# Kernel optimization log

Hardware: AMD Instinct MI355X
Metric: run time of the kernel (lower is better)

Reference implementation:

```python
import jax, jax.numpy as jnp
from jax import lax
import numpy as np

B, S, T = 64, 256, 256          # sentences, tokens, parser transitions per sentence
WDIMS, PDIMS = 128, 32
H = 256                          # per-direction hidden = ldims // 2
LDIMS = 2 * H
HID = 512
NRELS = 46
K, NNVECS = 3, 3
SLOTS = (K + 1) * NNVECS         # 12 gathered hidden vectors per transition
FEAT = LDIMS * SLOTS             # 6144 = hidLayer input dim
VW, VP = 40003, 53
ROUT = 2 * NRELS + 1             # 93


def _lstm(x, Wih, Whh, bih, bhh, reverse=False):
    """torch.nn.LSTMCell recurrence over seq axis. x: [B,S,D] -> h: [B,S,H]."""
    Bx = x.shape[0]
    Hh = Whh.shape[1]
    xs = jnp.swapaxes(x, 0, 1)  # [S,B,D]
    xg = xs @ Wih.T + (bih + bhh)  # precompute input gates [S,B,4H]

    def step(carry, g_in):
        h, c = carry
        g = g_in + h @ Whh.T
        i, f, gg, o = jnp.split(g, 4, axis=-1)
        i = jax.nn.sigmoid(i); f = jax.nn.sigmoid(f)
        gg = jnp.tanh(gg); o = jax.nn.sigmoid(o)
        c = f * c + i * gg
        h = o * jnp.tanh(c)
        return (h, c), h

    init = (jnp.zeros((Bx, Hh), x.dtype), jnp.zeros((Bx, Hh), x.dtype))
    _, hs = lax.scan(step, init, xg, reverse=reverse)
    return jnp.swapaxes(hs, 0, 1)  # [B,S,H], backward pass aligned to positions


def _forward(word_ids, pos_ids, feat_idx, wlookup, plookup,
             Wih1f, Whh1f, bih1f, bhh1f, Wih1b, Whh1b, bih1b, bhh1b,
             Wih2f, Whh2f, bih2f, bhh2f, Wih2b, Whh2b, bih2b, bhh2b,
             hidLayer, hidBias, outLayer, outBias,
             rhidLayer, rhidBias, routLayer, routBias):
    # token embeddings: ivec = cat(wordvec, posvec)
    ivec = jnp.concatenate([wlookup[word_ids], plookup[pos_ids]], axis=-1)  # [B,S,160]
    # first biLSTM
    f1 = _lstm(ivec, Wih1f, Whh1f, bih1f, bhh1f)
    b1 = _lstm(ivec, Wih1b, Whh1b, bih1b, bhh1b, reverse=True)
    vec1 = jnp.concatenate([f1, b1], axis=-1)  # [B,S,512]
    # second biLSTM (bibiFlag)
    f2 = _lstm(vec1, Wih2f, Whh2f, bih2f, bhh2f)
    b2 = _lstm(vec1, Wih2b, Whh2b, bih2b, bhh2b, reverse=True)
    vec = jnp.concatenate([f2, b2], axis=-1)  # [B,S,512]
    # __evaluate: concat (k+1)*nnvecs hidden vectors per transition
    bidx = jnp.arange(B)[:, None, None]
    feats = vec[bidx, feat_idx]                      # [B,T,12,512]
    feats = feats.reshape(B, T, FEAT)                # [B,T,6144]
    # unlabeled action scores: out = outLayer @ tanh(hidLayer @ input + hidBias) + outBias
    hid = jnp.tanh(jnp.einsum('btf,hf->bth', feats, hidLayer) + hidBias)
    out = jnp.einsum('bth,oh->bto', hid, outLayer) + outBias        # [B,T,3]
    # labeled relation scores
    rhid = jnp.tanh(jnp.einsum('btf,hf->bth', feats, rhidLayer) + rhidBias)
    rout = jnp.einsum('bth,oh->bto', rhid, routLayer) + routBias    # [B,T,93]
    return out, rout


def setup_inputs() -> dict:
    key = jax.random.key(0)
    ks = iter(jax.random.split(key, 40))

    def nrm(shape, scale=0.05):
        return jax.random.normal(next(ks), shape, jnp.float32) * scale

    inp = {}
    inp['word_ids'] = jax.random.randint(next(ks), (B, S), 0, VW)
    inp['pos_ids'] = jax.random.randint(next(ks), (B, S), 0, VP)
    inp['feat_idx'] = jax.random.randint(next(ks), (B, T, SLOTS), 0, S)
    inp['wlookup'] = nrm((VW, WDIMS))
    inp['plookup'] = nrm((VP, PDIMS))
    D1 = WDIMS + PDIMS
    for tag, din in (('1f', D1), ('1b', D1), ('2f', LDIMS), ('2b', LDIMS)):
        inp['Wih' + tag] = nrm((4 * H, din))
        inp['Whh' + tag] = nrm((4 * H, H))
        inp['bih' + tag] = nrm((4 * H,))
        inp['bhh' + tag] = nrm((4 * H,))
    inp['hidLayer'] = nrm((HID, FEAT), 0.02)
    inp['hidBias'] = nrm((HID,))
    inp['outLayer'] = nrm((3, HID))
    inp['outBias'] = nrm((3,))
    inp['rhidLayer'] = nrm((HID, FEAT), 0.02)
    inp['rhidBias'] = nrm((HID,))
    inp['routLayer'] = nrm((ROUT, HID))
    inp['routBias'] = nrm((ROUT,))
    return inp


def reference(word_ids, pos_ids, feat_idx, wlookup, plookup,
              Wih1f, Whh1f, bih1f, bhh1f, Wih1b, Whh1b, bih1b, bhh1b,
              Wih2f, Whh2f, bih2f, bhh2f, Wih2b, Whh2b, bih2b, bhh2b,
              hidLayer, hidBias, outLayer, outBias,
              rhidLayer, rhidBias, routLayer, routBias):
    return _forward(word_ids, pos_ids, feat_idx, wlookup, plookup,
                    Wih1f, Whh1f, bih1f, bhh1f, Wih1b, Whh1b, bih1b, bhh1b,
                    Wih2f, Whh2f, bih2f, bhh2f, Wih2b, Whh2b, bih2b, bhh2b,
                    hidLayer, hidBias, outLayer, outBias,
                    rhidLayer, rhidBias, routLayer, routBias)
```

## Files before the change

### kernel.cpp

```cpp
#include <hip/hip_runtime.h>
#include <hip/hip_fp16.h>
#include <math.h>


namespace {
constexpr int kB = 64, kS = 256, kH = 256, kG4 = 1024;
constexpr int kLD = 512;
constexpr int kTok = kB * kS;
}

typedef _Float16 h2 __attribute__((ext_vector_type(2)));
typedef _Float16 h4 __attribute__((ext_vector_type(4)));
typedef _Float16 h8 __attribute__((ext_vector_type(8)));
typedef float f4 __attribute__((ext_vector_type(4)));

#if __has_builtin(__builtin_amdgcn_fdot2)
#define USE_FDOT2 1
#else
#define USE_FDOT2 0
#endif

__device__ __forceinline__ float dot2acc(h2 w, h2 hh, float acc) {
#if USE_FDOT2
  return __builtin_amdgcn_fdot2(w, hh, acc, false);
#else
  return fmaf((float)w.x, (float)hh.x, fmaf((float)w.y, (float)hh.y, acc));
#endif
}

__device__ __forceinline__ void stage16(const void* g, void* lds_base, int lane) {
#if __has_builtin(__builtin_amdgcn_global_load_lds)
  (void)lane;
  __builtin_amdgcn_global_load_lds((const __attribute__((address_space(1))) void*)g,
                                   (__attribute__((address_space(3))) void*)lds_base,
                                   16, 0, 0);
#else
  *(uint4*)((char*)lds_base + lane * 16) = *(const uint4*)g;
#endif
}

__global__ void embed_h(const int* __restrict__ wid, const int* __restrict__ pid,
                        const float* __restrict__ wl, const float* __restrict__ pl,
                        _Float16* __restrict__ dst) {
  int tid = blockIdx.x * blockDim.x + threadIdx.x;
  if (tid >= kTok * 24) return;
  int tok = tid / 24, c8 = tid % 24;
  h8 o;
  if (c8 < 20) {
    const float* src = (c8 < 16) ? (wl + (size_t)wid[tok] * 128 + c8 * 8)
                                 : (pl + (size_t)pid[tok] * 32 + (c8 - 16) * 8);
    float4 v0 = *(const float4*)src;
    float4 v1 = *(const float4*)(src + 4);
    o[0] = (_Float16)v0.x; o[1] = (_Float16)v0.y;
    o[2] = (_Float16)v0.z; o[3] = (_Float16)v0.w;
    o[4] = (_Float16)v1.x; o[5] = (_Float16)v1.y;
    o[6] = (_Float16)v1.z; o[7] = (_Float16)v1.w;
  } else {
    o = (h8)(_Float16)0.f;
  }
  *(h8*)(dst + (size_t)tok * 192 + c8 * 8) = o;
}

__global__ void f2h_pad(const float* __restrict__ src, _Float16* __restrict__ dst,
                        int rows, int Kin, int Kpad) {
  int per = Kpad >> 2;
  int tid = blockIdx.x * blockDim.x + threadIdx.x;
  if (tid >= rows * per) return;
  int row = tid / per, c4 = (tid % per) << 2;
  h4 o;
  if (c4 < Kin) {
    float4 v = *(const float4*)(src + (size_t)row * Kin + c4);
    o[0] = (_Float16)v.x; o[1] = (_Float16)v.y;
    o[2] = (_Float16)v.z; o[3] = (_Float16)v.w;
  } else {
    o = (h4)(_Float16)0.f;
  }
  *(h4*)(dst + (size_t)row * Kpad + c4) = o;
}

__global__ void prep_bias(const float* __restrict__ b0, const float* __restrict__ b1,
                          const float* __restrict__ b2, const float* __restrict__ b3,
                          const float* __restrict__ b4, const float* __restrict__ b5,
                          const float* __restrict__ b6, const float* __restrict__ b7,
                          float* __restrict__ bsum) {
  int tid = blockIdx.x * blockDim.x + threadIdx.x;
  if (tid >= 4 * kG4) return;
  int grp = tid >> 10, i = tid & 1023;
  const float* x; const float* y;
  switch (grp) {
    case 0: x = b0; y = b1; break;
    case 1: x = b2; y = b3; break;
    case 2: x = b4; y = b5; break;
    default: x = b6; y = b7; break;
  }
  bsum[tid] = x[i] + y[i];
}

__global__ void concat_bias(const float* __restrict__ a, const float* __restrict__ b,
                            float* __restrict__ dst) {
  int tid = blockIdx.x * blockDim.x + threadIdx.x;
  if (tid >= kG4) return;
  dst[tid] = (tid < 512) ? a[tid] : b[tid - 512];
}

template <bool GATHER, bool TANH>
__global__ __launch_bounds__(256) void mfma_gemm(
    const _Float16* __restrict__ A, int lda,
    const _Float16* __restrict__ W,
    const float* __restrict__ bias,
    const _Float16* __restrict__ vsrc, const int* __restrict__ fidx,
    float* __restrict__ C, int K) {
  __shared__ _Float16 Asm[128 * 64];
  __shared__ _Float16 Bsm[128 * 64];
  const int tid = threadIdx.x;
  const int w = tid >> 6, l = tid & 63;
  const int wr = w >> 1, wc = w & 1;
  const int m0 = blockIdx.y * 128, n0 = blockIdx.x * 128;
  const int lrow = l & 15, lk8 = (l >> 4) << 3;
  const int stg_r = l >> 3;
  const int stg_c = (l & 7) ^ stg_r;

  f4 acc[4][4] = {};

  for (int k0 = 0; k0 < K; k0 += 64) {
#pragma unroll
    for (int ii = 0; ii < 4; ++ii) {
      const int r = w * 32 + ii * 8 + stg_r;
      const _Float16* ga;
      if (GATHER) {
        const int token = m0 + r;
        const int slot = k0 >> 9;
        const int idx = fidx[token * 12 + slot];
        ga = vsrc + ((((size_t)(token >> 8) << 8) + idx) << 9) + (k0 & 511) + (stg_c << 3);
      } else {
        ga = A + (size_t)(m0 + r) * lda + k0 + (stg_c << 3);
      }
      stage16(ga, &Asm[(size_t)(w * 32 + ii * 8) * 64], l);
      const _Float16* gb = W + (size_t)(n0 + r) * K + k0 + (stg_c << 3);
      stage16(gb, &Bsm[(size_t)(w * 32 + ii * 8) * 64], l);
    }
    __syncthreads();
#pragma unroll
    for (int kk = 0; kk < 64; kk += 32) {
      const int c0 = (kk + lk8) >> 3;
      h8 af[4], bf[4];
#pragma unroll
      for (int m = 0; m < 4; ++m) {
        const int row = wr * 64 + m * 16 + lrow;
        af[m] = *(const h8*)&Asm[row * 64 + ((c0 ^ (row & 7)) << 3)];
      }
#pragma unroll
      for (int n = 0; n < 4; ++n) {
        const int row = wc * 64 + n * 16 + lrow;
        bf[n] = *(const h8*)&Bsm[row * 64 + ((c0 ^ (row & 7)) << 3)];
      }
#pragma unroll
      for (int m = 0; m < 4; ++m)
#pragma unroll
        for (int n = 0; n < 4; ++n)
          acc[m][n] = __builtin_amdgcn_mfma_f32_16x16x32_f16(af[m], bf[n], acc[m][n], 0, 0, 0);
    }
    __syncthreads();
  }
#pragma unroll
  for (int n = 0; n < 4; ++n) {
    const int col = n0 + wc * 64 + n * 16 + lrow;
    const float bb = bias[col];
#pragma unroll
    for (int m = 0; m < 4; ++m) {
      const int rowb = m0 + wr * 64 + m * 16 + ((l >> 4) << 2);
#pragma unroll
      for (int r = 0; r < 4; ++r) {
        float v = acc[m][n][r] + bb;
        if (TANH) v = tanhf(v);
        C[(size_t)(rowb + r) * kG4 + col] = v;
      }
    }
  }
}

template <bool TANH>
__global__ __launch_bounds__(256) void gemm_kernel(
    const float* __restrict__ A, int lda,
    const float* __restrict__ W,
    const float* __restrict__ bias,
    float* __restrict__ C, int ldc, int N, int K) {
  __shared__ float As[8][128];
  __shared__ float Bs[8][128];
  const int tid = threadIdx.x;
  const int m0 = blockIdx.y * 128;
  const int n0 = blockIdx.x * 128;
  const int tx = tid & 15, ty = tid >> 4;
  const int lm = tid >> 1;
  const int lk = (tid & 1) * 4;
  float acc[8][8] = {};

  for (int k0 = 0; k0 < K; k0 += 8) {
    float4 av = *(const float4*)(A + (size_t)(m0 + lm) * lda + k0 + lk);
    const int n = n0 + lm;
    float4 bv = make_float4(0.f, 0.f, 0.f, 0.f);
    if (n < N) bv = *(const float4*)(W + (size_t)n * K + k0 + lk);
    __syncthreads();
    As[lk + 0][lm] = av.x; As[lk + 1][lm] = av.y;
    As[lk + 2][lm] = av.z; As[lk + 3][lm] = av.w;
    Bs[lk + 0][lm] = bv.x; Bs[lk + 1][lm] = bv.y;
    Bs[lk + 2][lm] = bv.z; Bs[lk + 3][lm] = bv.w;
    __syncthreads();
#pragma unroll
    for (int kk = 0; kk < 8; kk++) {
      float a[8], b8[8];
      *(float4*)&a[0]  = *(const float4*)&As[kk][ty * 8];
      *(float4*)&a[4]  = *(const float4*)&As[kk][ty * 8 + 4];
      *(float4*)&b8[0] = *(const float4*)&Bs[kk][tx * 8];
      *(float4*)&b8[4] = *(const float4*)&Bs[kk][tx * 8 + 4];
#pragma unroll
      for (int i = 0; i < 8; i++)
#pragma unroll
        for (int j = 0; j < 8; j++)
          acc[i][j] = fmaf(a[i], b8[j], acc[i][j]);
    }
  }
#pragma unroll
  for (int i = 0; i < 8; i++) {
    size_t m = m0 + ty * 8 + i;
#pragma unroll
    for (int j = 0; j < 8; j++) {
      int n = n0 + tx * 8 + j;
      if (n < N) {
        float v = acc[i][j] + bias[n];
        if (TANH) v = tanhf(v);
        C[m * ldc + n] = v;
      }
    }
  }
}

__global__ __launch_bounds__(512, 2) void lstm_rec_kernel(
    const float* __restrict__ xg_f, const float* __restrict__ xg_b,
    const float* __restrict__ Whh_f, const float* __restrict__ Whh_b,
    _Float16* __restrict__ out ) {
  __shared__ uint4 wlds4[16 * 512];
  __shared__ __align__(16) _Float16 hp_lds[kH];
  __shared__ float g_lds[kG4];

  const int bid = blockIdx.x;
  const int dir = bid & 1;
  const int row = bid >> 1;
  const float* xg  = dir ? xg_b : xg_f;
  const float* Whh = dir ? Whh_b : Whh_f;
  const int t = threadIdx.x;
  const int tsw = t ^ ((t >> 3) & 7);

  h2 wA[96], wB[96];
  const float2* r0 = (const float2*)(Whh + (size_t)(2 * t) * kH);
  const float2* r1 = (const float2*)(Whh + (size_t)(2 * t + 1) * kH);
#pragma unroll
  for (int j = 0; j < 96; ++j) {
    float2 w0 = r0[j]; wA[j].x = (_Float16)w0.x; wA[j].y = (_Float16)w0.y;
    float2 w1 = r1[j]; wB[j].x = (_Float16)w1.x; wB[j].y = (_Float16)w1.y;
  }
#pragma unroll
  for (int q = 0; q < 8; ++q) {
    unsigned int u0[4], u1[4];
#pragma unroll
    for (int p = 0; p < 4; ++p) {
      float2 f0 = r0[96 + 4 * q + p];
      float2 f1 = r1[96 + 4 * q + p];
      h2 a; a.x = (_Float16)f0.x; a.y = (_Float16)f0.y;
      h2 b; b.x = (_Float16)f1.x; b.y = (_Float16)f1.y;
      u0[p] = __builtin_bit_cast(unsigned int, a);
      u1[p] = __builtin_bit_cast(unsigned int, b);
    }
    wlds4[q * 512 + tsw]       = make_uint4(u0[0], u0[1], u0[2], u0[3]);
    wlds4[(8 + q) * 512 + tsw] = make_uint4(u1[0], u1[1], u1[2], u1[3]);
  }
  if (t < 32) ((uint4*)hp_lds)[t] = make_uint4(0, 0, 0, 0);
  float c_state = 0.f;
  __syncthreads();

  const uint4* hp4 = (const uint4*)hp_lds;
  const int s0 = dir ? (kS - 1) : 0;
  float2 xv = *(const float2*)(xg + ((size_t)(row * kS + s0)) * kG4 + 2 * t);

  for (int it = 0; it < kS; ++it) {
    const int s = dir ? (kS - 1 - it) : it;
    float a0e = xv.x, a1e = xv.y, a0o = 0.f, a1o = 0.f;
    float2 xv_next = make_float2(0.f, 0.f);
    if (it + 1 < kS) {
      const int sn = dir ? (kS - 2 - it) : (it + 1);
      xv_next = *(const float2*)(xg + ((size_t)(row * kS + sn)) * kG4 + 2 * t);
    }
#pragma unroll
    for (int j4 = 0; j4 < 24; ++j4) {
      uint4 hv = hp4[j4];
      h2 h0 = __builtin_bit_cast(h2, hv.x);
      h2 h1 = __builtin_bit_cast(h2, hv.y);
      h2 hh2 = __builtin_bit_cast(h2, hv.z);
      h2 h3 = __builtin_bit_cast(h2, hv.w);
      a0e = dot2acc(wA[4 * j4 + 0], h0, a0e);  a1e = dot2acc(wB[4 * j4 + 0], h0, a1e);
      a0o = dot2acc(wA[4 * j4 + 1], h1, a0o);  a1o = dot2acc(wB[4 * j4 + 1], h1, a1o);
      a0e = dot2acc(wA[4 * j4 + 2], hh2, a0e); a1e = dot2acc(wB[4 * j4 + 2], hh2, a1e);
      a0o = dot2acc(wA[4 * j4 + 3], h3, a0o);  a1o = dot2acc(wB[4 * j4 + 3], h3, a1o);
    }
#pragma unroll
    for (int q = 0; q < 8; ++q) {
      uint4 hv = hp4[24 + q];
      uint4 w0v = wlds4[q * 512 + tsw];
      uint4 w1v = wlds4[(8 + q) * 512 + tsw];
      h2 h0 = __builtin_bit_cast(h2, hv.x);
      h2 h1 = __builtin_bit_cast(h2, hv.y);
      h2 hh2 = __builtin_bit_cast(h2, hv.z);
      h2 h3 = __builtin_bit_cast(h2, hv.w);
      a0e = dot2acc(__builtin_bit_cast(h2, w0v.x), h0, a0e);
      a1e = dot2acc(__builtin_bit_cast(h2, w1v.x), h0, a1e);
      a0o = dot2acc(__builtin_bit_cast(h2, w0v.y), h1, a0o);
      a1o = dot2acc(__builtin_bit_cast(h2, w1v.y), h1, a1o);
      a0e = dot2acc(__builtin_bit_cast(h2, w0v.z), hh2, a0e);
      a1e = dot2acc(__builtin_bit_cast(h2, w1v.z), hh2, a1e);
      a0o = dot2acc(__builtin_bit_cast(h2, w0v.w), h3, a0o);
      a1o = dot2acc(__builtin_bit_cast(h2, w1v.w), h3, a1o);
    }
    ((float2*)g_lds)[t] = make_float2(a0e + a0o, a1e + a1o);
    __syncthreads();
    if (t < kH) {
      float gi = g_lds[t];
      float gf = g_lds[t + 256];
      float gg = g_lds[t + 512];
      float go = g_lds[t + 768];
      float i_ = 1.f / (1.f + __expf(-gi));
      float f_ = 1.f / (1.f + __expf(-gf));
      float g_ = tanhf(gg);
      float o_ = 1.f / (1.f + __expf(-go));
      c_state = f_ * c_state + i_ * g_;
      float h = o_ * tanhf(c_state);
      hp_lds[t] = (_Float16)h;
      out[((size_t)(row * kS + s)) * kLD + dir * kH + t] = (_Float16)h;
    }
    __syncthreads();
    xv = xv_next;
  }
}

extern "C" void kernel_launch(void* const* d_in, const int* in_sizes, int n_in,
                              void* d_out, int out_size, void* d_ws, size_t ws_size,
                              hipStream_t stream) {
  const int*   word_ids = (const int*)d_in[0];
  const int*   pos_ids  = (const int*)d_in[1];
  const int*   feat_idx = (const int*)d_in[2];
  const float* wlookup  = (const float*)d_in[3];
  const float* plookup  = (const float*)d_in[4];
  const float* Wih1f = (const float*)d_in[5];
  const float* Whh1f = (const float*)d_in[6];
  const float* bih1f = (const float*)d_in[7];
  const float* bhh1f = (const float*)d_in[8];
  const float* Wih1b = (const float*)d_in[9];
  const float* Whh1b = (const float*)d_in[10];
  const float* bih1b = (const float*)d_in[11];
  const float* bhh1b = (const float*)d_in[12];
  const float* Wih2f = (const float*)d_in[13];
  const float* Whh2f = (const float*)d_in[14];
  const float* bih2f = (const float*)d_in[15];
  const float* bhh2f = (const float*)d_in[16];
  const float* Wih2b = (const float*)d_in[17];
  const float* Whh2b = (const float*)d_in[18];
  const float* bih2b = (const float*)d_in[19];
  const float* bhh2b = (const float*)d_in[20];
  const float* hidLayer  = (const float*)d_in[21];
  const float* hidBias   = (const float*)d_in[22];
  const float* outLayer  = (const float*)d_in[23];
  const float* outBias   = (const float*)d_in[24];
  const float* rhidLayer = (const float*)d_in[25];
  const float* rhidBias  = (const float*)d_in[26];
  const float* routLayer = (const float*)d_in[27];
  const float* routBias  = (const float*)d_in[28];

  float* ws = (float*)d_ws;
  const size_t F_IVECH = 0;
  const size_t F_XGF   = F_IVECH + (size_t)kTok * 192 / 2;
  const size_t F_XGB   = F_XGF + (size_t)kTok * kG4;
  const size_t F_V1H   = F_XGB + (size_t)kTok * kG4;
  const size_t F_V2H   = F_V1H + (size_t)kTok * kLD / 2;
  const size_t F_WHA   = F_V2H + (size_t)kTok * kLD / 2;
  const size_t F_WHB   = F_WHA + (size_t)2 * kG4 * 192 / 2;
  const size_t F_WHID  = F_WHB + (size_t)2 * kG4 * 512 / 2;
  const size_t F_BSUM  = F_WHID + (size_t)kG4 * 6144 / 2;
  const size_t F_HB    = F_BSUM + 4 * kG4;
  const size_t F_END   = F_HB + kG4;
  const size_t F_HID   = F_XGF;
  if (ws_size < F_END * sizeof(float)) return;

  _Float16* ivec_h = (_Float16*)(ws + F_IVECH);
  float*    xg_f   = ws + F_XGF;
  float*    xg_b   = ws + F_XGB;
  _Float16* vec1h  = (_Float16*)(ws + F_V1H);
  _Float16* vec2h  = (_Float16*)(ws + F_V2H);
  _Float16* whA    = (_Float16*)(ws + F_WHA);
  _Float16* whB    = (_Float16*)(ws + F_WHB);
  _Float16* whid   = (_Float16*)(ws + F_WHID);
  float*    bsum   = ws + F_BSUM;
  float*    hb     = ws + F_HB;
  float*    hidc   = ws + F_HID;
  float*    outp   = (float*)d_out;

  prep_bias<<<16, 256, 0, stream>>>(bih1f, bhh1f, bih1b, bhh1b,
                                    bih2f, bhh2f, bih2b, bhh2b, bsum);
  concat_bias<<<4, 256, 0, stream>>>(hidBias, rhidBias, hb);
  f2h_pad<<<(1024 * 48 + 255) / 256, 256, 0, stream>>>(Wih1f, whA, 1024, 160, 192);
  f2h_pad<<<(1024 * 48 + 255) / 256, 256, 0, stream>>>(Wih1b, whA + 1024 * 192, 1024, 160, 192);
  f2h_pad<<<(1024 * 128 + 255) / 256, 256, 0, stream>>>(Wih2f, whB, 1024, 512, 512);
  f2h_pad<<<(1024 * 128 + 255) / 256, 256, 0, stream>>>(Wih2b, whB + 1024 * 512, 1024, 512, 512);
  f2h_pad<<<(512 * 1536 + 255) / 256, 256, 0, stream>>>(hidLayer, whid, 512, 6144, 6144);
  f2h_pad<<<(512 * 1536 + 255) / 256, 256, 0, stream>>>(rhidLayer, whid + (size_t)512 * 6144,
                                                        512, 6144, 6144);
  embed_h<<<(kTok * 24 + 255) / 256, 256, 0, stream>>>(word_ids, pos_ids,
                                                       wlookup, plookup, ivec_h);
  mfma_gemm<false, false><<<dim3(8, 128), 256, 0, stream>>>(
      ivec_h, 192, whA, bsum + 0, nullptr, nullptr, xg_f, 192);
  mfma_gemm<false, false><<<dim3(8, 128), 256, 0, stream>>>(
      ivec_h, 192, whA + 1024 * 192, bsum + 1024, nullptr, nullptr, xg_b, 192);
  lstm_rec_kernel<<<128, 512, 0, stream>>>(xg_f, xg_b, Whh1f, Whh1b, vec1h);
  mfma_gemm<false, false><<<dim3(8, 128), 256, 0, stream>>>(
      vec1h, 512, whB, bsum + 2048, nullptr, nullptr, xg_f, 512);
  mfma_gemm<false, false><<<dim3(8, 128), 256, 0, stream>>>(
      vec1h, 512, whB + 1024 * 512, bsum + 3072, nullptr, nullptr, xg_b, 512);
  lstm_rec_kernel<<<128, 512, 0, stream>>>(xg_f, xg_b, Whh2f, Whh2b, vec2h);
  mfma_gemm<true, true><<<dim3(8, 128), 256, 0, stream>>>(
      nullptr, 0, whid, hb, vec2h, feat_idx, hidc, 6144);
  gemm_kernel<false><<<dim3(1, 128), 256, 0, stream>>>(
      hidc, kG4, outLayer, outBias, outp, 3, 3, 512);
  gemm_kernel<false><<<dim3(1, 128), 256, 0, stream>>>(
      hidc + 512, kG4, routLayer, routBias, outp + (size_t)kTok * 3, 93, 93, 512);
}
```

Measured before the change: 1.791 ms.

## Restructure LSTM recurrence so thread pairs own all four gates of a unit

The recurrent kernel now assigns each pair of threads one hidden unit across all four gates, with the K dimension split in half between the two threads. A shuffle reduction replaces the gate exchange through shared memory, and a double-buffered h vector allows one barrier per timestep instead of two. The gate nonlinearities also switch to exp plus fast reciprocal approximations. This aims to cut per-step barrier and LDS round-trip latency on the serial path, at some cost in accuracy from the approximate tanh and sigmoid and in duplicated activation math across the thread pair.

```diff
diff --git a/kernel.cpp b/kernel.cpp
--- a/kernel.cpp
+++ b/kernel.cpp
@@ -26,6 +26,19 @@
 #else
   return fmaf((float)w.x, (float)hh.x, fmaf((float)w.y, (float)hh.y, acc));
 #endif
+}
+
+__device__ __forceinline__ float fastrcp(float x) {
+#if __has_builtin(__builtin_amdgcn_rcpf)
+  return __builtin_amdgcn_rcpf(x);
+#else
+  return 1.f / x;
+#endif
+}
+__device__ __forceinline__ float sigf(float x) { return fastrcp(1.f + __expf(-x)); }
+__device__ __forceinline__ float tanhfast(float x) {
+  float u = __expf(2.f * x);
+  return 1.f - 2.f * fastrcp(u + 1.f);
 }
 
 __device__ __forceinline__ void stage16(const void* g, void* lds_base, int lane) {
@@ -240,8 +253,7 @@
     const float* __restrict__ Whh_f, const float* __restrict__ Whh_b,
     _Float16* __restrict__ out ) {
   __shared__ uint4 wlds4[16 * 512];
-  __shared__ __align__(16) _Float16 hp_lds[kH];
-  __shared__ float g_lds[kG4];
+  __shared__ __align__(16) _Float16 hbuf[2][kH];
 
   const int bid = blockIdx.x;
   const int dir = bid & 1;
@@ -249,95 +261,116 @@
   const float* xg  = dir ? xg_b : xg_f;
   const float* Whh = dir ? Whh_b : Whh_f;
   const int t = threadIdx.x;
-  const int tsw = t ^ ((t >> 3) & 7);
-
-  h2 wA[96], wB[96];
-  const float2* r0 = (const float2*)(Whh + (size_t)(2 * t) * kH);
-  const float2* r1 = (const float2*)(Whh + (size_t)(2 * t + 1) * kH);
-#pragma unroll
-  for (int j = 0; j < 96; ++j) {
-    float2 w0 = r0[j]; wA[j].x = (_Float16)w0.x; wA[j].y = (_Float16)w0.y;
-    float2 w1 = r1[j]; wB[j].x = (_Float16)w1.x; wB[j].y = (_Float16)w1.y;
-  }
-#pragma unroll
-  for (int q = 0; q < 8; ++q) {
-    unsigned int u0[4], u1[4];
-#pragma unroll
-    for (int p = 0; p < 4; ++p) {
-      float2 f0 = r0[96 + 4 * q + p];
-      float2 f1 = r1[96 + 4 * q + p];
-      h2 a; a.x = (_Float16)f0.x; a.y = (_Float16)f0.y;
-      h2 b; b.x = (_Float16)f1.x; b.y = (_Float16)f1.y;
-      u0[p] = __builtin_bit_cast(unsigned int, a);
-      u1[p] = __builtin_bit_cast(unsigned int, b);
-    }
-    wlds4[q * 512 + tsw]       = make_uint4(u0[0], u0[1], u0[2], u0[3]);
-    wlds4[(8 + q) * 512 + tsw] = make_uint4(u1[0], u1[1], u1[2], u1[3]);
-  }
-  if (t < 32) ((uint4*)hp_lds)[t] = make_uint4(0, 0, 0, 0);
+  const int c  = t >> 1;
+  const int kh = t & 1;
+  const int kbase = kh * 128;
+
+  h2 wv[4][48];
+#pragma unroll
+  for (int g = 0; g < 4; ++g) {
+    const float2* wr = (const float2*)(Whh + (size_t)(g * kH + c) * kH + kbase);
+#pragma unroll
+    for (int p = 0; p < 48; ++p) {
+      float2 f = wr[p];
+      h2 a; a.x = (_Float16)f.x; a.y = (_Float16)f.y;
+      wv[g][p] = a;
+    }
+#pragma unroll
+    for (int q = 0; q < 4; ++q) {
+      unsigned u[4];
+#pragma unroll
+      for (int i = 0; i < 4; ++i) {
+        float2 f = wr[48 + 4 * q + i];
+        h2 a; a.x = (_Float16)f.x; a.y = (_Float16)f.y;
+        u[i] = __builtin_bit_cast(unsigned, a);
+      }
+      wlds4[(g * 4 + q) * 512 + t] = make_uint4(u[0], u[1], u[2], u[3]);
+    }
+  }
+  if (t < kH) hbuf[1][t] = (_Float16)0.f;
   float c_state = 0.f;
   __syncthreads();
 
-  const uint4* hp4 = (const uint4*)hp_lds;
-  const int s0 = dir ? (kS - 1) : 0;
-  float2 xv = *(const float2*)(xg + ((size_t)(row * kS + s0)) * kG4 + 2 * t);
+  const float* xgr = xg + (size_t)(row * kS) * kG4;
+  const int sstep = dir ? -1 : 1;
+  int s = dir ? (kS - 1) : 0;
+  float x0 = xgr[(size_t)s * kG4 + c];
+  float x1 = xgr[(size_t)s * kG4 + c + 256];
+  float x2 = xgr[(size_t)s * kG4 + c + 512];
+  float x3 = xgr[(size_t)s * kG4 + c + 768];
 
   for (int it = 0; it < kS; ++it) {
-    const int s = dir ? (kS - 1 - it) : it;
-    float a0e = xv.x, a1e = xv.y, a0o = 0.f, a1o = 0.f;
-    float2 xv_next = make_float2(0.f, 0.f);
-    if (it + 1 < kS) {
-      const int sn = dir ? (kS - 2 - it) : (it + 1);
-      xv_next = *(const float2*)(xg + ((size_t)(row * kS + sn)) * kG4 + 2 * t);
-    }
-#pragma unroll
-    for (int j4 = 0; j4 < 24; ++j4) {
-      uint4 hv = hp4[j4];
+    int sn = s + sstep; sn = sn < 0 ? 0 : (sn > kS - 1 ? kS - 1 : sn);
+    const float* xnrow = xgr + (size_t)sn * kG4 + c;
+    float xn0 = xnrow[0], xn1 = xnrow[256], xn2 = xnrow[512], xn3 = xnrow[768];
+
+    float a0 = kh ? 0.f : x0;
+    float a1 = kh ? 0.f : x1;
+    float a2 = kh ? 0.f : x2;
+    float a3 = kh ? 0.f : x3;
+
+    const uint4* hh = ((const uint4*)hbuf[(it & 1) ^ 1]) + kh * 16;
+#pragma unroll
+    for (int u = 0; u < 12; ++u) {
+      uint4 hv = hh[u];
       h2 h0 = __builtin_bit_cast(h2, hv.x);
       h2 h1 = __builtin_bit_cast(h2, hv.y);
-      h2 hh2 = __builtin_bit_cast(h2, hv.z);
+      h2 hx = __builtin_bit_cast(h2, hv.z);
       h2 h3 = __builtin_bit_cast(h2, hv.w);
-      a0e = dot2acc(wA[4 * j4 + 0], h0, a0e);  a1e = dot2acc(wB[4 * j4 + 0], h0, a1e);
-      a0o = dot2acc(wA[4 * j4 + 1], h1, a0o);  a1o = dot2acc(wB[4 * j4 + 1], h1, a1o);
-      a0e = dot2acc(wA[4 * j4 + 2], hh2, a0e); a1e = dot2acc(wB[4 * j4 + 2], hh2, a1e);
-      a0o = dot2acc(wA[4 * j4 + 3], h3, a0o);  a1o = dot2acc(wB[4 * j4 + 3], h3, a1o);
-    }
-#pragma unroll
-    for (int q = 0; q < 8; ++q) {
-      uint4 hv = hp4[24 + q];
-      uint4 w0v = wlds4[q * 512 + tsw];
-      uint4 w1v = wlds4[(8 + q) * 512 + tsw];
+      a0 = dot2acc(wv[0][4*u+0], h0, a0); a0 = dot2acc(wv[0][4*u+1], h1, a0);
+      a0 = dot2acc(wv[0][4*u+2], hx, a0); a0 = dot2acc(wv[0][4*u+3], h3, a0);
+      a1 = dot2acc(wv[1][4*u+0], h0, a1); a1 = dot2acc(wv[1][4*u+1], h1, a1);
+      a1 = dot2acc(wv[1][4*u+2], hx, a1); a1 = dot2acc(wv[1][4*u+3], h3, a1);
+      a2 = dot2acc(wv[2][4*u+0], h0, a2); a2 = dot2acc(wv[2][4*u+1], h1, a2);
+      a2 = dot2acc(wv[2][4*u+2], hx, a2); a2 = dot2acc(wv[2][4*u+3], h3, a2);
+      a3 = dot2acc(wv[3][4*u+0], h0, a3); a3 = dot2acc(wv[3][4*u+1], h1, a3);
+      a3 = dot2acc(wv[3][4*u+2], hx, a3); a3 = dot2acc(wv[3][4*u+3], h3, a3);
+    }
+#pragma unroll
+    for (int q = 0; q < 4; ++q) {
+      uint4 hv = hh[12 + q];
       h2 h0 = __builtin_bit_cast(h2, hv.x);
       h2 h1 = __builtin_bit_cast(h2, hv.y);
-      h2 hh2 = __builtin_bit_cast(h2, hv.z);
+      h2 hx = __builtin_bit_cast(h2, hv.z);
       h2 h3 = __builtin_bit_cast(h2, hv.w);
-      a0e = dot2acc(__builtin_bit_cast(h2, w0v.x), h0, a0e);
-      a1e = dot2acc(__builtin_bit_cast(h2, w1v.x), h0, a1e);
-      a0o = dot2acc(__builtin_bit_cast(h2, w0v.y), h1, a0o);
-      a1o = dot2acc(__builtin_bit_cast(h2, w1v.y), h1, a1o);
-      a0e = dot2acc(__builtin_bit_cast(h2, w0v.z), hh2, a0e);
-      a1e = dot2acc(__builtin_bit_cast(h2, w1v.z), hh2, a1e);
-      a0o = dot2acc(__builtin_bit_cast(h2, w0v.w), h3, a0o);
-      a1o = dot2acc(__builtin_bit_cast(h2, w1v.w), h3, a1o);
-    }
-    ((float2*)g_lds)[t] = make_float2(a0e + a0o, a1e + a1o);
+      uint4 w0 = wlds4[(0 * 4 + q) * 512 + t];
+      uint4 w1 = wlds4[(1 * 4 + q) * 512 + t];
+      uint4 w2 = wlds4[(2 * 4 + q) * 512 + t];
+      uint4 w3 = wlds4[(3 * 4 + q) * 512 + t];
+      a0 = dot2acc(__builtin_bit_cast(h2, w0.x), h0, a0);
+      a0 = dot2acc(__builtin_bit_cast(h2, w0.y), h1, a0);
+      a0 = dot2acc(__builtin_bit_cast(h2, w0.z), hx, a0);
+      a0 = dot2acc(__builtin_bit_cast(h2, w0.w), h3, a0);
+      a1 = dot2acc(__builtin_bit_cast(h2, w1.x), h0, a1);
+      a1 = dot2acc(__builtin_bit_cast(h2, w1.y), h1, a1);
+      a1 = dot2acc(__builtin_bit_cast(h2, w1.z), hx, a1);
+      a1 = dot2acc(__builtin_bit_cast(h2, w1.w), h3, a1);
+      a2 = dot2acc(__builtin_bit_cast(h2, w2.x), h0, a2);
+      a2 = dot2acc(__builtin_bit_cast(h2, w2.y), h1, a2);
+      a2 = dot2acc(__builtin_bit_cast(h2, w2.z), hx, a2);
+      a2 = dot2acc(__builtin_bit_cast(h2, w2.w), h3, a2);
+      a3 = dot2acc(__builtin_bit_cast(h2, w3.x), h0, a3);
+      a3 = dot2acc(__builtin_bit_cast(h2, w3.y), h1, a3);
+      a3 = dot2acc(__builtin_bit_cast(h2, w3.z), hx, a3);
+      a3 = dot2acc(__builtin_bit_cast(h2, w3.w), h3, a3);
+    }
+    float s0 = a0 + __shfl_xor(a0, 1);
+    float s1 = a1 + __shfl_xor(a1, 1);
+    float s2 = a2 + __shfl_xor(a2, 1);
+    float s3 = a3 + __shfl_xor(a3, 1);
+    float i_ = sigf(s0);
+    float f_ = sigf(s1);
+    float g_ = tanhfast(s2);
+    float o_ = sigf(s3);
+    c_state = f_ * c_state + i_ * g_;
+    float h = o_ * tanhfast(c_state);
+    if (!kh) {
+      hbuf[it & 1][c] = (_Float16)h;
+      out[((size_t)(row * kS + s)) * kLD + dir * kH + c] = (_Float16)h;
+    }
+    s += sstep;
     __syncthreads();
-    if (t < kH) {
-      float gi = g_lds[t];
-      float gf = g_lds[t + 256];
-      float gg = g_lds[t + 512];
-      float go = g_lds[t + 768];
-      float i_ = 1.f / (1.f + __expf(-gi));
-      float f_ = 1.f / (1.f + __expf(-gf));
-      float g_ = tanhf(gg);
-      float o_ = 1.f / (1.f + __expf(-go));
-      c_state = f_ * c_state + i_ * g_;
-      float h = o_ * tanhf(c_state);
-      hp_lds[t] = (_Float16)h;
-      out[((size_t)(row * kS + s)) * kLD + dir * kH + t] = (_Float16)h;
-    }
-    __syncthreads();
-    xv = xv_next;
+    x0 = xn0; x1 = xn1; x2 = xn2; x3 = xn3;
   }
 }
 
```

Measured after the change: 1.663 ms. 7.1% less time.
